# Performance work log

Measured on AMD Instinct MI355X. Metric: run time of the kernel, lower is better.

## Reference

```python
import jax, jax.numpy as jnp
import numpy as np

T, B, D = 512, 64, 1024

def setup_inputs() -> dict:
    key = jax.random.key(0)
    k1, k2 = jax.random.split(key)
    goal = jax.random.normal(k1, (T, B, D), dtype=jnp.float32)
    init_goal_state = jax.random.normal(k2, (1, B, D), dtype=jnp.float32)
    return {"goal": goal, "init_goal_state": init_goal_state}

def reference(goal, init_goal_state):
    # state_t = init + sum_{i<=t} goal_i  (prefix sum over time), out_t = sigmoid(state_t)
    states = init_goal_state[0][None] + jnp.cumsum(goal, axis=0)  # [T, B, D]
    outputs = jax.nn.sigmoid(states)
    final_state = states[-1][None]  # [1, B, D]
    return (outputs, (final_state, final_state))
```

## Files before the change

### kernel.cpp

```cpp
#include <hip/hip_runtime.h>

#define T_DIM   512
#define BD      65536
#define BD4     16384
#define CHUNKS  16
#define CHUNK_T 32

typedef float nfloat4 __attribute__((ext_vector_type(4)));

__device__ __forceinline__ float sigmoid_fast(float x) {
    float e = __expf(-x);
    return __builtin_amdgcn_rcpf(1.0f + e);
}

__global__ __launch_bounds__(256)
void SumGoalHistory_chunksums(const float4* __restrict__ goal,
                              float4* __restrict__ sums) {
    int gid = blockIdx.x * 256 + threadIdx.x;
    int c = gid >> 14;
    int i = gid & (BD4 - 1);
    const float4* p = goal + (size_t)c * CHUNK_T * BD4 + i;
    float sx = 0.f, sy = 0.f, sz = 0.f, sw = 0.f;
    #pragma unroll 8
    for (int t = 0; t < CHUNK_T; ++t) {
        float4 v = p[(size_t)t * BD4];
        sx += v.x; sy += v.y; sz += v.z; sw += v.w;
    }
    sums[c * BD4 + i] = make_float4(sx, sy, sz, sw);
}

__global__ __launch_bounds__(256)
void SumGoalHistory_scan(const float4* __restrict__ goal,
                         const float4* __restrict__ init,
                         const float4* __restrict__ sums,
                         float4* __restrict__ out) {
    int gid = blockIdx.x * 256 + threadIdx.x;
    int c = gid >> 14;
    int i = gid & (BD4 - 1);

    float4 a = init[i];
    float ax = a.x, ay = a.y, az = a.z, aw = a.w;
    for (int cc = 0; cc < c; ++cc) {
        float4 s = sums[cc * BD4 + i];
        ax += s.x; ay += s.y; az += s.z; aw += s.w;
    }

    const float4* p = goal + (size_t)c * CHUNK_T * BD4 + i;
    nfloat4*      o = (nfloat4*)out + (size_t)c * CHUNK_T * BD4 + i;
    #pragma unroll 4
    for (int t = 0; t < CHUNK_T; ++t) {
        float4 v = p[(size_t)t * BD4];
        ax += v.x; ay += v.y; az += v.z; aw += v.w;
        nfloat4 r;
        r.x = sigmoid_fast(ax);
        r.y = sigmoid_fast(ay);
        r.z = sigmoid_fast(az);
        r.w = sigmoid_fast(aw);
        __builtin_nontemporal_store(r, o + (size_t)t * BD4);
    }

    if (c == CHUNKS - 1) {
        float4 f = make_float4(ax, ay, az, aw);
        float4* fin = out + (size_t)T_DIM * BD4;
        fin[i] = f;
        fin[BD4 + i] = f;
    }
}

extern "C" void kernel_launch(void* const* d_in, const int* in_sizes, int n_in,
                              void* d_out, int out_size, void* d_ws, size_t ws_size,
                              hipStream_t stream) {
    const float4* goal = (const float4*)d_in[0];
    const float4* init = (const float4*)d_in[1];
    float4* out  = (float4*)d_out;
    float4* sums = (float4*)d_ws;

    SumGoalHistory_chunksums<<<(CHUNKS - 1) * BD4 / 256, 256, 0, stream>>>(goal, sums);
    SumGoalHistory_scan<<<CHUNKS * BD4 / 256, 256, 0, stream>>>(goal, init, sums, out);
}
```

Before: 251.7 us.

## Fuse chunk-sum and scan kernels into a single decoupled lookback kernel

Merges the two-pass chunk-sum and scan into one kernel. Blocks get virtual IDs in launch order from an atomic counter, publish their chunk sums with release flags, and spin on the flags of earlier chunks before running the local scan with sigmoid. Each block reads its goal chunk twice within the same kernel, so the second read can hit cache. This removes a separate launch and the global barrier between passes, at the cost of an extra tiny init kernel and spin-wait synchronization.

```diff
diff --git a/kernel.cpp b/kernel.cpp
--- a/kernel.cpp
+++ b/kernel.cpp
@@ -1,10 +1,11 @@
 #include <hip/hip_runtime.h>
 
 #define T_DIM   512
-#define BD      65536
 #define BD4     16384
 #define CHUNKS  16
 #define CHUNK_T 32
+#define CB      64
+#define NBLOCKS (CHUNKS * CB)
 
 typedef float nfloat4 __attribute__((ext_vector_type(4)));
 
@@ -14,11 +15,25 @@
 }
 
 __global__ __launch_bounds__(256)
-void SumGoalHistory_chunksums(const float4* __restrict__ goal,
-                              float4* __restrict__ sums) {
-    int gid = blockIdx.x * 256 + threadIdx.x;
-    int c = gid >> 14;
-    int i = gid & (BD4 - 1);
+void SumGoalHistory_init(unsigned* __restrict__ ws) {
+    for (int k = threadIdx.x; k < 1024; k += 256) ws[k] = 0u;
+}
+
+__global__ __launch_bounds__(256)
+void SumGoalHistory_fused(const float4* __restrict__ goal,
+                          const float4* __restrict__ init,
+                          float4* __restrict__ out,
+                          unsigned* __restrict__ ctr,
+                          unsigned* __restrict__ flags,
+                          float4* __restrict__ sums) {
+    __shared__ unsigned s_vid;
+    if (threadIdx.x == 0) s_vid = atomicAdd(ctr, 1u);
+    __syncthreads();
+    const unsigned vid = s_vid;
+    const int c = vid >> 6;
+    const int j = vid & (CB - 1);
+    const int i = j * 256 + threadIdx.x;
+
     const float4* p = goal + (size_t)c * CHUNK_T * BD4 + i;
     float sx = 0.f, sy = 0.f, sz = 0.f, sw = 0.f;
     #pragma unroll 8
@@ -26,27 +41,28 @@
         float4 v = p[(size_t)t * BD4];
         sx += v.x; sy += v.y; sz += v.z; sw += v.w;
     }
-    sums[c * BD4 + i] = make_float4(sx, sy, sz, sw);
-}
 
-__global__ __launch_bounds__(256)
-void SumGoalHistory_scan(const float4* __restrict__ goal,
-                         const float4* __restrict__ init,
-                         const float4* __restrict__ sums,
-                         float4* __restrict__ out) {
-    int gid = blockIdx.x * 256 + threadIdx.x;
-    int c = gid >> 14;
-    int i = gid & (BD4 - 1);
+    if (c < CHUNKS - 1) {
+        sums[(size_t)c * BD4 + i] = make_float4(sx, sy, sz, sw);
+        __threadfence();
+        __syncthreads();
+        if (threadIdx.x == 0)
+            __hip_atomic_store(&flags[vid], 1u,
+                               __ATOMIC_RELEASE, __HIP_MEMORY_SCOPE_AGENT);
+    }
 
     float4 a = init[i];
     float ax = a.x, ay = a.y, az = a.z, aw = a.w;
     for (int cc = 0; cc < c; ++cc) {
-        float4 s = sums[cc * BD4 + i];
+        const unsigned f = cc * CB + j;
+        while (__hip_atomic_load(&flags[f],
+                                 __ATOMIC_ACQUIRE, __HIP_MEMORY_SCOPE_AGENT) == 0u)
+            __builtin_amdgcn_s_sleep(1);
+        float4 s = sums[(size_t)cc * BD4 + i];
         ax += s.x; ay += s.y; az += s.z; aw += s.w;
     }
 
-    const float4* p = goal + (size_t)c * CHUNK_T * BD4 + i;
-    nfloat4*      o = (nfloat4*)out + (size_t)c * CHUNK_T * BD4 + i;
+    nfloat4* o = (nfloat4*)out + (size_t)c * CHUNK_T * BD4 + i;
     #pragma unroll 4
     for (int t = 0; t < CHUNK_T; ++t) {
         float4 v = p[(size_t)t * BD4];
@@ -60,10 +76,10 @@
     }
 
     if (c == CHUNKS - 1) {
-        float4 f = make_float4(ax, ay, az, aw);
+        float4 fv = make_float4(ax, ay, az, aw);
         float4* fin = out + (size_t)T_DIM * BD4;
-        fin[i] = f;
-        fin[BD4 + i] = f;
+        fin[i] = fv;
+        fin[BD4 + i] = fv;
     }
 }
 
@@ -72,9 +88,13 @@
                               hipStream_t stream) {
     const float4* goal = (const float4*)d_in[0];
     const float4* init = (const float4*)d_in[1];
-    float4* out  = (float4*)d_out;
-    float4* sums = (float4*)d_ws;
+    float4* out = (float4*)d_out;
 
-    SumGoalHistory_chunksums<<<(CHUNKS - 1) * BD4 / 256, 256, 0, stream>>>(goal, sums);
-    SumGoalHistory_scan<<<CHUNKS * BD4 / 256, 256, 0, stream>>>(goal, init, sums, out);
+    unsigned* ctr   = (unsigned*)d_ws;
+    unsigned* flags = (unsigned*)((char*)d_ws + 256);
+    float4*   sums  = (float4*)((char*)d_ws + 4096);
+
+    SumGoalHistory_init<<<1, 256, 0, stream>>>((unsigned*)d_ws);
+    SumGoalHistory_fused<<<NBLOCKS, 256, 0, stream>>>(goal, init, out,
+                                                      ctr, flags, sums);
 }
```

Measured after the change: 687.6 us. +173.2%, slower.
